# Performance work log

Hardware: AMD Instinct MI355X
Metric: run time of the kernel (lower is better)

The kernel has to match this reference:

```python
import jax, jax.numpy as jnp
import numpy as np
import math

N_HEADS = 8
INPUT_DIM = 128
EMBED_DIM = 128
KEY_DIM = EMBED_DIM // N_HEADS  # 16, val_dim == key_dim
B = 4
N = 1024


def setup_inputs() -> dict:
    key = jax.random.key(0)
    ks = jax.random.split(key, 12)
    def unif(k, shape):
        stdv = 1.0 / math.sqrt(shape[-1])
        return jax.random.uniform(k, shape, jnp.float32, -stdv, stdv)
    return {
        "q": jax.random.normal(ks[0], (B, N, INPUT_DIM), jnp.float32),
        "out_source_attn": jax.random.normal(ks[1], (N_HEADS, B, N, N), jnp.float32),
        "st_edge": jax.random.normal(ks[2], (N_HEADS, B, N, N), jnp.float32),
        "W_query": unif(ks[3], (N_HEADS, INPUT_DIM, KEY_DIM)),
        "W_key": unif(ks[4], (N_HEADS, INPUT_DIM, KEY_DIM)),
        "W_val": unif(ks[5], (N_HEADS, INPUT_DIM, KEY_DIM)),
        "w1": unif(ks[6], (8, 16)),  # Linear(16, 8) weight
        "b1": unif(ks[7], (8,)),
        "w2": unif(ks[8], (8, 8)),   # Linear(8, 8) weight
        "b2": unif(ks[9], (8,)),
        "W_out": unif(ks[10], (N_HEADS, KEY_DIM, EMBED_DIM)),
    }


def reference(q, out_source_attn, st_edge, W_query, W_key, W_val, w1, b1, w2, b2, W_out):
    norm = 1.0 / math.sqrt(KEY_DIM)
    # per-head projections: (h, B, N, k)
    Q = jnp.einsum('bni,hik->hbnk', q, W_query)
    K = jnp.einsum('bni,hik->hbnk', q, W_key)
    V = jnp.einsum('bni,hiv->hbnv', q, W_val)
    # compatibility scores + spatio-temporal edge bias, scaled
    compat = (jnp.einsum('hbnk,hbmk->hbnm', Q, K) + st_edge) * norm
    # concat on head axis -> (16, B, N, N)
    scores = jnp.concatenate([compat, out_source_attn], axis=0)
    # tiny per-position MLP over the 16 concatenated channels
    x = scores.transpose(1, 2, 3, 0)                 # (B, N, N, 16)
    x = jax.nn.relu(x @ w1.T + b1)                   # (B, N, N, 8)
    x = x @ w2.T + b2                                # (B, N, N, 8)
    attn_logits = x.transpose(3, 0, 1, 2)            # (8, B, N, N)
    attn = jax.nn.softmax(attn_logits, axis=-1)
    heads = jnp.einsum('hbnm,hbmv->hbnv', attn, V)   # (8, B, N, v)
    out = jnp.einsum('hbnv,hve->bne', heads, W_out)  # (B, N, embed)
    return (out, out_source_attn, st_edge)
```

## Files before the change

### kernel.cpp

```cpp
#include <hip/hip_runtime.h>

typedef _Float16 half_t;
typedef _Float16 half2_t __attribute__((ext_vector_type(2)));
typedef float f4 __attribute__((ext_vector_type(4)));

#define BB 4
#define NN 1024
#define NH 8
#define KD 16
#define ID 128
#define NT 4
#define LGR 520

static constexpr size_t OUT_SZ   = (size_t)BB * NN * 128;
static constexpr size_t ATT_SZ   = (size_t)NH * BB * NN * NN;
static constexpr size_t OFF_OSS  = OUT_SZ;
static constexpr size_t OFF_ST   = OUT_SZ + ATT_SZ;
static constexpr size_t HSTRIDE  = (size_t)BB * NN * NN;

__device__ __forceinline__ float fdot2u(unsigned int a, unsigned int b, float c) {
    union { unsigned int u; half2_t h; } ua, ub;
    ua.u = a; ub.u = b;
    return __builtin_amdgcn_fdot2(ua.h, ub.h, c, false);
}

__device__ __forceinline__ void lds_barrier() {
    asm volatile("s_waitcnt lgkmcnt(0)\n\ts_barrier" ::: "memory");
}

__global__ __launch_bounds__(128) void qkv_kernel(
    const float* __restrict__ q,  const float* __restrict__ Wq,
    const float* __restrict__ Wk, const float* __restrict__ Wv,
    half_t* __restrict__ Qh, half_t* __restrict__ Kp, half_t* __restrict__ Vp)
{
    const int bn = blockIdx.x;
    const int j  = threadIdx.x;
    const int h  = j >> 4, k = j & 15;
    const int b  = bn >> 10, n = bn & 1023;

    __shared__ float qrow[ID];
    qrow[j] = q[(size_t)bn * ID + j];
    __syncthreads();

    const float* wq = Wq + h * ID * KD + k;
    const float* wk = Wk + h * ID * KD + k;
    const float* wv = Wv + h * ID * KD + k;
    float aq = 0.f, ak = 0.f, av = 0.f;
#pragma unroll
    for (int i = 0; i < ID; ++i) {
        float x = qrow[i];
        aq = fmaf(x, wq[i * KD], aq);
        ak = fmaf(x, wk[i * KD], ak);
        av = fmaf(x, wv[i * KD], av);
    }
    Qh[(size_t)bn * 128 + j] = (half_t)aq;
    const size_t pr = ((size_t)((b * NH + h) * 8 + (k >> 1)) * NN + n) * 2 + (k & 1);
    Kp[pr] = (half_t)ak;
    Vp[pr] = (half_t)av;
}

__global__ __launch_bounds__(256) void vtrans_kernel(
    const unsigned int* __restrict__ Vp, half_t* __restrict__ Vt)
{
    const int bh  = blockIdx.x >> 2;
    const int nt  = blockIdx.x & 3;
    const int tid = threadIdx.x;
    const int n0  = nt * 256;

    __shared__ half_t t[16][264];

#pragma unroll
    for (int vp = 0; vp < 8; ++vp) {
        union { unsigned int u; half_t h2[2]; } c;
        c.u = Vp[((size_t)(bh * 8 + vp)) * NN + n0 + tid];
        t[2 * vp + 0][tid] = c.h2[0];
        t[2 * vp + 1][tid] = c.h2[1];
    }
    __syncthreads();
#pragma unroll
    for (int rep = 0; rep < 2; ++rep) {
        const int cch = tid + rep * 256;
        const int row = cch >> 5, col = (cch & 31) * 8;
        const uint4 vv = *reinterpret_cast<const uint4*>(&t[row][col]);
        *reinterpret_cast<uint4*>(Vt + ((size_t)(bh * 16 + row)) * NN + n0 + col) = vv;
    }
}

__global__ __launch_bounds__(512, 4) void fused_kernel(
    const float* __restrict__ oss, const float* __restrict__ st,
    const half_t* __restrict__ Qh, const unsigned int* __restrict__ Kp,
    const half_t* __restrict__ Vt,
    const float* __restrict__ w1,  const float* __restrict__ b1,
    const float* __restrict__ w2,  const float* __restrict__ b2,
    const float* __restrict__ Wout, float* __restrict__ out)
{
    const int n0  = blockIdx.x * NT;
    const int b   = blockIdx.y;
    const int tid = threadIdx.x;
    const int rg  = tid >> 7;
    const int t7  = tid & 127;
    const int mi0 = t7 * 4;

    __shared__ __align__(16) unsigned int kst[8 * 512];
    __shared__ __align__(16) half_t lg[NT * NH * LGR];
    __shared__ unsigned int qsh[NT][64];
    __shared__ float wsumPart[8][NH];
    __shared__ float headsSh[NT][128];

    if (tid < 256) qsh[tid >> 6][tid & 63] =
        reinterpret_cast<const unsigned int*>(Qh + ((size_t)(b * NN + n0 + (tid >> 6))) * 128)[tid & 63];
    if (tid < 64) wsumPart[tid >> 3][tid & 7] = 0.f;
    __syncthreads();

    const int ph   = tid >> 6;
    const int pv   = (tid >> 2) & 15;
    const int psub = tid & 3;

    float pvAcc[NT] = {0.f, 0.f, 0.f, 0.f};

#pragma unroll 1
    for (int hf = 0; hf < 2; ++hf) {
        float y[4][8];
#pragma unroll
        for (int mo = 0; mo < 4; ++mo)
#pragma unroll
            for (int o = 0; o < 8; ++o) y[mo][o] = b1[o];

#pragma unroll 1
        for (int h = 0; h < NH; ++h) {
            lds_barrier();
            {
                const int kp = tid >> 6, c = (tid & 63) * 8;
                const unsigned int* src =
                    Kp + ((size_t)((b * NH + h) * 8 + kp)) * NN + hf * 512 + c;
                const uint4 A  = *reinterpret_cast<const uint4*>(src);
                const uint4 B2 = *reinterpret_cast<const uint4*>(src + 4);
                *reinterpret_cast<uint4*>(&kst[kp * 512 + c])     = A;
                *reinterpret_cast<uint4*>(&kst[kp * 512 + c + 4]) = B2;
            }
            lds_barrier();

            const size_t idx = (size_t)h * HSTRIDE +
                ((size_t)(b * NN + n0 + rg)) * NN + hf * 512 + mi0;
            const f4 sv = __builtin_nontemporal_load(reinterpret_cast<const f4*>(st + idx));
            const f4 ov = __builtin_nontemporal_load(reinterpret_cast<const f4*>(oss + idx));
            *reinterpret_cast<f4*>(out + OFF_ST + idx)  = sv;
            *reinterpret_cast<f4*>(out + OFF_OSS + idx) = ov;
            const float svv[4] = {sv.x, sv.y, sv.z, sv.w};
            const float ovv[4] = {ov.x, ov.y, ov.z, ov.w};

            float acc[4] = {0.f, 0.f, 0.f, 0.f};
#pragma unroll
            for (int kp = 0; kp < 8; ++kp) {
                const uint4 k4 = *reinterpret_cast<const uint4*>(&kst[kp * 512 + mi0]);
                const unsigned int qp = qsh[rg][h * 8 + kp];
                acc[0] = fdot2u(k4.x, qp, acc[0]);
                acc[1] = fdot2u(k4.y, qp, acc[1]);
                acc[2] = fdot2u(k4.z, qp, acc[2]);
                acc[3] = fdot2u(k4.w, qp, acc[3]);
            }

            float w1c[8], w1o[8];
#pragma unroll
            for (int o = 0; o < 8; ++o) { w1c[o] = w1[o * 16 + h]; w1o[o] = w1[o * 16 + 8 + h]; }
#pragma unroll
            for (int mo = 0; mo < 4; ++mo) {
                const float c = (acc[mo] + svv[mo]) * 0.25f;
#pragma unroll
                for (int o = 0; o < 8; ++o)
                    y[mo][o] = fmaf(c, w1c[o], fmaf(ovv[mo], w1o[o], y[mo][o]));
            }
        }

        float lgv[8][4];
#pragma unroll
        for (int mo = 0; mo < 4; ++mo) {
            float z[8];
#pragma unroll
            for (int o = 0; o < 8; ++o) z[o] = fmaxf(y[mo][o], 0.f);
#pragma unroll
            for (int p = 0; p < 8; ++p) {
                float a = b2[p];
#pragma unroll
                for (int o = 0; o < 8; ++o) a = fmaf(z[o], w2[p * 8 + o], a);
                lgv[p][mo] = a;
            }
        }
        float psum[8];
#pragma unroll
        for (int p = 0; p < 8; ++p) {
            const float e0 = __expf(lgv[p][0]);
            const float e1 = __expf(lgv[p][1]);
            const float e2 = __expf(lgv[p][2]);
            const float e3 = __expf(lgv[p][3]);
            psum[p] = (e0 + e1) + (e2 + e3);
            union { uint2 u; half_t h4[4]; } w;
            w.h4[0] = (half_t)e0; w.h4[1] = (half_t)e1;
            w.h4[2] = (half_t)e2; w.h4[3] = (half_t)e3;
            *reinterpret_cast<uint2*>(&lg[(rg * NH + p) * LGR + mi0]) = w.u;
        }
#pragma unroll
        for (int p = 0; p < 8; ++p)
#pragma unroll
            for (int s = 32; s > 0; s >>= 1)
                psum[p] += __shfl_xor(psum[p], s);
        if ((tid & 63) == 0) {
            const int w = tid >> 6;
#pragma unroll
            for (int p = 0; p < 8; ++p) wsumPart[w][p] += psum[p];
        }
        lds_barrier();

        {
            const unsigned int* vr = reinterpret_cast<const unsigned int*>(
                Vt + ((size_t)((b * NH + ph) * KD + pv)) * NN + hf * 512);
#pragma unroll 2
            for (int c2 = 0; c2 < 16; ++c2) {
                const int mo = (c2 * 4 + psub) * 8;
                const uint4 vv = *reinterpret_cast<const uint4*>(vr + mo / 2);
#pragma unroll
                for (int r = 0; r < NT; ++r) {
                    const uint4 ww = *reinterpret_cast<const uint4*>(&lg[(r * NH + ph) * LGR + mo]);
                    pvAcc[r] = fdot2u(vv.x, ww.x, pvAcc[r]);
                    pvAcc[r] = fdot2u(vv.y, ww.y, pvAcc[r]);
                    pvAcc[r] = fdot2u(vv.z, ww.z, pvAcc[r]);
                    pvAcc[r] = fdot2u(vv.w, ww.w, pvAcc[r]);
                }
            }
        }
        lds_barrier();
    }

#pragma unroll
    for (int r = 0; r < NT; ++r) {
        pvAcc[r] += __shfl_xor(pvAcc[r], 1);
        pvAcc[r] += __shfl_xor(pvAcc[r], 2);
    }
    if (psub == 0) {
#pragma unroll
        for (int r = 0; r < NT; ++r) {
            const float s = wsumPart[2 * r][ph] + wsumPart[2 * r + 1][ph];
            headsSh[r][ph * 16 + pv] = pvAcc[r] * (1.0f / s);
        }
    }
    __syncthreads();

    {
        const int e  = tid & 127;
        const int q2 = tid >> 7;
        float a[NT] = {0.f, 0.f, 0.f, 0.f};
#pragma unroll
        for (int ii = 0; ii < 32; ++ii) {
            const int i = q2 * 32 + ii;
            const float wr = Wout[(size_t)i * 128 + e];
#pragma unroll
            for (int r = 0; r < NT; ++r) a[r] = fmaf(headsSh[r][i], wr, a[r]);
        }
        float* red = reinterpret_cast<float*>(kst);
#pragma unroll
        for (int r = 0; r < NT; ++r) red[(q2 * NT + r) * 128 + e] = a[r];
        __syncthreads();
        {
            const int r = tid >> 7, e2 = tid & 127;
            out[((size_t)(b * NN + n0 + r)) * 128 + e2] =
                red[(0 * NT + r) * 128 + e2] + red[(1 * NT + r) * 128 + e2] +
                red[(2 * NT + r) * 128 + e2] + red[(3 * NT + r) * 128 + e2];
        }
    }
}

extern "C" void kernel_launch(void* const* d_in, const int* in_sizes, int n_in,
                              void* d_out, int out_size, void* d_ws, size_t ws_size,
                              hipStream_t stream) {
    const float* q    = (const float*)d_in[0];
    const float* oss  = (const float*)d_in[1];
    const float* st   = (const float*)d_in[2];
    const float* Wq   = (const float*)d_in[3];
    const float* Wk   = (const float*)d_in[4];
    const float* Wv   = (const float*)d_in[5];
    const float* w1   = (const float*)d_in[6];
    const float* b1   = (const float*)d_in[7];
    const float* w2   = (const float*)d_in[8];
    const float* b2   = (const float*)d_in[9];
    const float* Wout = (const float*)d_in[10];
    float* out = (float*)d_out;

    half_t* Qh = (half_t*)d_ws;
    half_t* Kp = (half_t*)((char*)d_ws + 1u * 1024u * 1024u);
    half_t* Vp = (half_t*)((char*)d_ws + 2u * 1024u * 1024u);
    half_t* Vt = (half_t*)((char*)d_ws + 3u * 1024u * 1024u);

    qkv_kernel<<<dim3(BB * NN), dim3(128), 0, stream>>>(q, Wq, Wk, Wv, Qh, Kp, Vp);
    vtrans_kernel<<<dim3(32 * 4), dim3(256), 0, stream>>>((const unsigned int*)Vp, Vt);
    fused_kernel<<<dim3(NN / NT, BB), dim3(512), 0, stream>>>(
        oss, st, Qh, (const unsigned int*)Kp, Vt,
        w1, b1, w2, b2, Wout, out);
}
```

Baseline: 147.8 us.

## Split K staging into two LDS halves and prefetch next head's K

Splits the per-head K tile in shared memory into two 4-pair halves. The second half and the next head's first half are loaded from global memory while dot products run on the half already resident, so global K loads overlap with compute rather than sitting between two barriers. The copy-through stores of st and oss are moved later in the loop body, and some __syncthreads calls become lds_barrier. This keeps the same number of barriers per head but holds more registers live, and it depends on lds_barrier being correct for global-to-LDS ordering.

```diff
diff --git a/kernel.cpp b/kernel.cpp
--- a/kernel.cpp
+++ b/kernel.cpp
@@ -101,7 +101,7 @@
     const int t7  = tid & 127;
     const int mi0 = t7 * 4;
 
-    __shared__ __align__(16) unsigned int kst[8 * 512];
+    __shared__ __align__(16) unsigned int kst[2][4 * 512];
     __shared__ __align__(16) half_t lg[NT * NH * LGR];
     __shared__ unsigned int qsh[NT][64];
     __shared__ float wsumPart[8][NH];
@@ -110,12 +110,15 @@
     if (tid < 256) qsh[tid >> 6][tid & 63] =
         reinterpret_cast<const unsigned int*>(Qh + ((size_t)(b * NN + n0 + (tid >> 6))) * 128)[tid & 63];
     if (tid < 64) wsumPart[tid >> 3][tid & 7] = 0.f;
-    __syncthreads();
+    lds_barrier();
 
     const int ph   = tid >> 6;
     const int pv   = (tid >> 2) & 15;
     const int psub = tid & 3;
 
+    const int skp = tid >> 7;
+    const int sc  = (tid & 127) * 4;
+
     float pvAcc[NT] = {0.f, 0.f, 0.f, 0.f};
 
 #pragma unroll 1
@@ -126,40 +129,58 @@
 #pragma unroll
             for (int o = 0; o < 8; ++o) y[mo][o] = b1[o];
 
+        {
+            const unsigned int* src =
+                Kp + ((size_t)((b * NH + 0) * 8 + skp)) * NN + hf * 512 + sc;
+            *reinterpret_cast<uint4*>(&kst[0][skp * 512 + sc]) =
+                *reinterpret_cast<const uint4*>(src);
+        }
+        lds_barrier();
+
 #pragma unroll 1
         for (int h = 0; h < NH; ++h) {
-            lds_barrier();
-            {
-                const int kp = tid >> 6, c = (tid & 63) * 8;
-                const unsigned int* src =
-                    Kp + ((size_t)((b * NH + h) * 8 + kp)) * NN + hf * 512 + c;
-                const uint4 A  = *reinterpret_cast<const uint4*>(src);
-                const uint4 B2 = *reinterpret_cast<const uint4*>(src + 4);
-                *reinterpret_cast<uint4*>(&kst[kp * 512 + c])     = A;
-                *reinterpret_cast<uint4*>(&kst[kp * 512 + c + 4]) = B2;
-            }
-            lds_barrier();
-
             const size_t idx = (size_t)h * HSTRIDE +
                 ((size_t)(b * NN + n0 + rg)) * NN + hf * 512 + mi0;
+
             const f4 sv = __builtin_nontemporal_load(reinterpret_cast<const f4*>(st + idx));
             const f4 ov = __builtin_nontemporal_load(reinterpret_cast<const f4*>(oss + idx));
-            *reinterpret_cast<f4*>(out + OFF_ST + idx)  = sv;
-            *reinterpret_cast<f4*>(out + OFF_OSS + idx) = ov;
-            const float svv[4] = {sv.x, sv.y, sv.z, sv.w};
-            const float ovv[4] = {ov.x, ov.y, ov.z, ov.w};
+            const unsigned int* srcO =
+                Kp + ((size_t)((b * NH + h) * 8 + 4 + skp)) * NN + hf * 512 + sc;
+            const uint4 kO = *reinterpret_cast<const uint4*>(srcO);
 
             float acc[4] = {0.f, 0.f, 0.f, 0.f};
 #pragma unroll
-            for (int kp = 0; kp < 8; ++kp) {
-                const uint4 k4 = *reinterpret_cast<const uint4*>(&kst[kp * 512 + mi0]);
+            for (int kp = 0; kp < 4; ++kp) {
+                const uint4 k4 = *reinterpret_cast<const uint4*>(&kst[0][kp * 512 + mi0]);
                 const unsigned int qp = qsh[rg][h * 8 + kp];
                 acc[0] = fdot2u(k4.x, qp, acc[0]);
                 acc[1] = fdot2u(k4.y, qp, acc[1]);
                 acc[2] = fdot2u(k4.z, qp, acc[2]);
                 acc[3] = fdot2u(k4.w, qp, acc[3]);
             }
-
+            *reinterpret_cast<uint4*>(&kst[1][skp * 512 + sc]) = kO;
+            lds_barrier();
+
+            uint4 kE;
+            if (h < 7) {
+                const unsigned int* srcE =
+                    Kp + ((size_t)((b * NH + h + 1) * 8 + skp)) * NN + hf * 512 + sc;
+                kE = *reinterpret_cast<const uint4*>(srcE);
+            }
+#pragma unroll
+            for (int kp = 0; kp < 4; ++kp) {
+                const uint4 k4 = *reinterpret_cast<const uint4*>(&kst[1][kp * 512 + mi0]);
+                const unsigned int qp = qsh[rg][h * 8 + 4 + kp];
+                acc[0] = fdot2u(k4.x, qp, acc[0]);
+                acc[1] = fdot2u(k4.y, qp, acc[1]);
+                acc[2] = fdot2u(k4.z, qp, acc[2]);
+                acc[3] = fdot2u(k4.w, qp, acc[3]);
+            }
+
+            *reinterpret_cast<f4*>(out + OFF_ST + idx)  = sv;
+            *reinterpret_cast<f4*>(out + OFF_OSS + idx) = ov;
+            const float svv[4] = {sv.x, sv.y, sv.z, sv.w};
+            const float ovv[4] = {ov.x, ov.y, ov.z, ov.w};
             float w1c[8], w1o[8];
 #pragma unroll
             for (int o = 0; o < 8; ++o) { w1c[o] = w1[o * 16 + h]; w1o[o] = w1[o * 16 + 8 + h]; }
@@ -170,6 +191,9 @@
                 for (int o = 0; o < 8; ++o)
                     y[mo][o] = fmaf(c, w1c[o], fmaf(ovv[mo], w1o[o], y[mo][o]));
             }
+            if (h < 7)
+                *reinterpret_cast<uint4*>(&kst[0][skp * 512 + sc]) = kE;
+            lds_barrier();
         }
 
         float lgv[8][4];
@@ -243,7 +267,7 @@
             headsSh[r][ph * 16 + pv] = pvAcc[r] * (1.0f / s);
         }
     }
-    __syncthreads();
+    lds_barrier();
 
     {
         const int e  = tid & 127;
@@ -259,7 +283,7 @@
         float* red = reinterpret_cast<float*>(kst);
 #pragma unroll
         for (int r = 0; r < NT; ++r) red[(q2 * NT + r) * 128 + e] = a[r];
-        __syncthreads();
+        lds_barrier();
         {
             const int r = tid >> 7, e2 = tid & 127;
             out[((size_t)(b * NN + n0 + r)) * 128 + e2] =
```

Result: slower. 152.2 us (+2.9%).
